# Optimization experiments

Measured on AMD Instinct MI355X. Metric: run time of the kernel, lower is better.

The kernel has to match this reference:

```python
import jax, jax.numpy as jnp
import numpy as np

HEADS = 8
DIM_HEAD = 128
EPS = 1e-5


def layer_norm(t, gamma):
    mu = jnp.mean(t, axis=-1, keepdims=True)
    var = jnp.var(t, axis=-1, keepdims=True)
    return (t - mu) / jnp.sqrt(var + EPS) * gamma


def setup_inputs() -> dict:
    key = jax.random.key(0)
    k1, k2, k3 = jax.random.split(key, 3)
    B, N, T, D = 16, 256, 4096, 1024
    img_queries = jax.random.normal(k1, (B, N, D), dtype=jnp.float32)
    x = jax.random.normal(k2, (B, T, D), dtype=jnp.float32)
    gamma_q = jnp.ones((D,), dtype=jnp.float32)
    gamma_x = jnp.ones((D,), dtype=jnp.float32)
    W_kv = jax.random.normal(k3, (D, 2 * DIM_HEAD), dtype=jnp.float32) * 0.02
    return {"img_queries": img_queries, "x": x, "gamma_q": gamma_q,
            "gamma_x": gamma_x, "W_kv": W_kv}


def reference(img_queries, x, gamma_q, gamma_x, W_kv):
    B, N, D = img_queries.shape
    scale = DIM_HEAD ** -0.5
    q_n = layer_norm(img_queries, gamma_q)            # [B,N,D]
    x_n = layer_norm(x, gamma_x)                      # [B,T,D]
    # b n (h d) -> b h n d
    q = q_n.reshape(B, N, HEADS, DIM_HEAD).transpose(0, 2, 1, 3)
    kv = x_n @ W_kv                                   # [B,T,2*dim_head]
    k = kv[..., :DIM_HEAD]                            # shared single K head; v chunk unused
    sim = jnp.einsum('bhid,bjd->bhij', q * scale, k)  # [B,H,N,T]
    sim = sim - jnp.max(sim, axis=-1, keepdims=True)
    attn = jax.nn.softmax(sim, axis=-1)
    out = jnp.einsum('bhij,bjf->bhif', attn, x_n)     # V = raw normed x, [B,H,N,D]
    # b h n f -> b (n h f)
    out = out.transpose(0, 2, 1, 3).reshape(B, N * HEADS * D)
    return out, attn
```

## Files before the change

### kernel.cpp

```cpp
#include <hip/hip_runtime.h>

typedef unsigned short u16;
typedef unsigned int u32;
typedef __attribute__((ext_vector_type(8))) short short8;
typedef __attribute__((ext_vector_type(4))) float f32x4;
typedef __attribute__((ext_vector_type(4))) unsigned int u32x4;

#define SCALE 0.08838834764831845f
#define OUT_ELEMS 33554432ull

__device__ __forceinline__ u16 f2b(float f) {
  u32 u = __float_as_uint(f);
  u32 r = u + 0x7fffu + ((u >> 16) & 1u);
  return (u16)(r >> 16);
}

__device__ __forceinline__ u32 cvtpk(float lo, float hi) {
  u32 r;
  asm("v_cvt_pk_bf16_f32 %0, %1, %2" : "=v"(r) : "v"(lo), "v"(hi));
  return r;
}

__device__ __forceinline__ void gload16(const void* g, void* l) {
  __builtin_amdgcn_global_load_lds((const __attribute__((address_space(1))) void*)g,
                                   (__attribute__((address_space(3))) void*)l, 16, 0, 0);
}

__device__ __forceinline__ uint2 shflx2(uint2 v, int m) {
  uint2 r;
  r.x = __shfl_xor(v.x, m, 64);
  r.y = __shfl_xor(v.y, m, 64);
  return r;
}

__global__ __launch_bounds__(256) void ln_rows(const float* __restrict__ in,
                                               const float* __restrict__ gamma,
                                               u16* __restrict__ out, float scale) {
  const int row = blockIdx.x;
  const int t = threadIdx.x;
  const float4 v = *(const float4*)(in + (size_t)row * 1024 + t * 4);
  float s = v.x + v.y + v.z + v.w;
  float q = v.x * v.x + v.y * v.y + v.z * v.z + v.w * v.w;
#pragma unroll
  for (int m = 32; m; m >>= 1) {
    s += __shfl_down(s, m);
    q += __shfl_down(q, m);
  }
  __shared__ float red[8];
  const int w = t >> 6;
  if ((t & 63) == 0) { red[w] = s; red[4 + w] = q; }
  __syncthreads();
  s = red[0] + red[1] + red[2] + red[3];
  q = red[4] + red[5] + red[6] + red[7];
  const float mu = s * (1.0f / 1024.0f);
  const float var = q * (1.0f / 1024.0f) - mu * mu;
  const float rs = rsqrtf(var + 1e-5f) * scale;
  const float4 g = *(const float4*)(gamma + t * 4);
  ushort4 o;
  o.x = f2b((v.x - mu) * rs * g.x);
  o.y = f2b((v.y - mu) * rs * g.y);
  o.z = f2b((v.z - mu) * rs * g.z);
  o.w = f2b((v.w - mu) * rs * g.w);
  *(ushort4*)(out + (size_t)row * 1024 + t * 4) = o;
}

__global__ __launch_bounds__(256) void cvt_w(const float* __restrict__ w, u16* __restrict__ wt) {
  const int n = blockIdx.x;
  const int t = threadIdx.x;
  const int d = t * 4;
  ushort4 o;
  o.x = f2b(w[(size_t)(d + 0) * 256 + n]);
  o.y = f2b(w[(size_t)(d + 1) * 256 + n]);
  o.z = f2b(w[(size_t)(d + 2) * 256 + n]);
  o.w = f2b(w[(size_t)(d + 3) * 256 + n]);
  *(ushort4*)(wt + (size_t)n * 1024 + d) = o;
}

__global__ __launch_bounds__(256) void transpose_xn(const u16* __restrict__ xn,
                                                    u16* __restrict__ xnt) {
  const int jt = blockIdx.x, dt = blockIdx.y, b = blockIdx.z;
  __shared__ u16 tile[64][72];
  const int t = threadIdx.x;
  const size_t src = ((size_t)b * 4096 + jt * 64) * 1024 + dt * 64;
#pragma unroll
  for (int p = 0; p < 2; ++p) {
    const int idx = t + 256 * p;
    const int j = idx >> 3, c = idx & 7;
    *(short8*)(&tile[j][c * 8]) = *(const short8*)(xn + src + (size_t)j * 1024 + c * 8);
  }
  __syncthreads();
  const size_t dst = ((size_t)b * 1024 + dt * 64) * 4096 + jt * 64;
#pragma unroll
  for (int p = 0; p < 2; ++p) {
    const int idx = t + 256 * p;
    const int d = idx >> 3, jj = idx & 7;
    short8 o;
#pragma unroll
    for (int e = 0; e < 8; ++e) o[e] = (short)tile[jj * 8 + e][d];
    *(short8*)(xnt + dst + (size_t)d * 4096 + jj * 8) = o;
  }
}

__global__ __launch_bounds__(256) void kgemm(const u16* __restrict__ xn,
                                             const u16* __restrict__ wt,
                                             u16* __restrict__ ks) {
  __shared__ u16 As[128 * 32];
  __shared__ u16 Bs[128 * 32];
  const int t = threadIdx.x;
  const int lane = t & 63, w = t >> 6;
  const int wm = w >> 1, wn = w & 1;
  const int j0 = blockIdx.x * 128;
  const int g = lane >> 4, r16 = lane & 15;
  f32x4 acc[4][4] = {};
  for (int k0 = 0; k0 < 1024; k0 += 32) {
    __syncthreads();
#pragma unroll
    for (int i = 0; i < 2; ++i) {
      const int seg = i * 4 + w;
      const int off = seg * 1024 + lane * 16;
      const int row = off >> 6;
      const int c = (off >> 4) & 3;
      const int sw = c ^ ((row >> 1) & 3);
      gload16(xn + ((size_t)(j0 + row)) * 1024 + k0 + sw * 8, (char*)As + seg * 1024);
      gload16(wt + ((size_t)row) * 1024 + k0 + sw * 8, (char*)Bs + seg * 1024);
    }
    __syncthreads();
    short8 a[4], bq[4];
#pragma unroll
    for (int mt = 0; mt < 4; ++mt) {
      const int row = wm * 64 + mt * 16 + r16;
      const int sw = g ^ ((row >> 1) & 3);
      a[mt] = *(const short8*)(As + row * 32 + sw * 8);
    }
#pragma unroll
    for (int nt = 0; nt < 4; ++nt) {
      const int row = wn * 64 + nt * 16 + r16;
      const int sw = g ^ ((row >> 1) & 3);
      bq[nt] = *(const short8*)(Bs + row * 32 + sw * 8);
    }
#pragma unroll
    for (int mt = 0; mt < 4; ++mt)
#pragma unroll
      for (int nt = 0; nt < 4; ++nt)
        acc[mt][nt] = __builtin_amdgcn_mfma_f32_16x16x32_bf16(a[mt], bq[nt], acc[mt][nt], 0, 0, 0);
  }
#pragma unroll
  for (int mt = 0; mt < 4; ++mt)
#pragma unroll
    for (int nt = 0; nt < 4; ++nt)
#pragma unroll
      for (int r = 0; r < 4; ++r) {
        const int j = j0 + wm * 64 + mt * 16 + g * 4 + r;
        const int n = wn * 64 + nt * 16 + r16;
        ks[(size_t)j * 128 + n] = f2b(acc[mt][nt][r]);
      }
}

__global__ __launch_bounds__(1024) void attn_kernel(const u16* __restrict__ qs,
                                                    const u16* __restrict__ ks,
                                                    float* __restrict__ attn,
                                                    u16* __restrict__ attnb) {
  const int blk = blockIdx.x;
  const int it = blk & 15, h = (blk >> 4) & 7, b = blk >> 7;
  const int i0 = it * 16;
  const int t = threadIdx.x;
  const int lane = t & 63, w = t >> 6;
  const int g = lane >> 4, r16 = lane & 15;
  __shared__ u16 Q[16 * 128];
  __shared__ float redm[256];
  __shared__ float reds[256];
  if (t < 256) {
    const int row = t >> 4, c = t & 15;
    const int sw = c ^ (row & 7);
    *(short8*)(Q + row * 128 + sw * 8) =
        *(const short8*)(qs + ((size_t)(b * 256 + i0 + row)) * 1024 + h * 128 + c * 8);
  }
  __syncthreads();
  short8 a[4];
#pragma unroll
  for (int kp = 0; kp < 4; ++kp) {
    const int c = kp * 4 + g;
    const int sw = c ^ (r16 & 7);
    a[kp] = *(const short8*)(Q + r16 * 128 + sw * 8);
  }
  const u16* kb = ks + (size_t)b * 4096 * 128;
  const int j0 = w * 256;
  f32x4 acc[16] = {};
#pragma unroll
  for (int kp = 0; kp < 4; ++kp) {
#pragma unroll
    for (int nt = 0; nt < 16; ++nt) {
      const short8 bv = *(const short8*)(kb + (size_t)(j0 + nt * 16 + r16) * 128 + kp * 32 + g * 8);
      acc[nt] = __builtin_amdgcn_mfma_f32_16x16x32_bf16(bv, a[kp], acc[nt], 0, 0, 0);
    }
  }
  float mx = acc[0][0];
#pragma unroll
  for (int nt = 0; nt < 16; ++nt)
#pragma unroll
    for (int r = 0; r < 4; ++r) mx = fmaxf(mx, acc[nt][r]);
  mx = fmaxf(mx, __shfl_xor(mx, 16));
  mx = fmaxf(mx, __shfl_xor(mx, 32));
  if (lane < 16) redm[w * 16 + lane] = mx;
  __syncthreads();
  float m = redm[r16];
#pragma unroll
  for (int w2 = 1; w2 < 16; ++w2) m = fmaxf(m, redm[w2 * 16 + r16]);
  float sm = 0.f;
#pragma unroll
  for (int nt = 0; nt < 16; ++nt)
#pragma unroll
    for (int r = 0; r < 4; ++r) {
      const float p = __expf(acc[nt][r] - m);
      acc[nt][r] = p;
      sm += p;
    }
  sm += __shfl_xor(sm, 16);
  sm += __shfl_xor(sm, 32);
  if (lane < 16) reds[w * 16 + lane] = sm;
  __syncthreads();
  float s = reds[r16];
#pragma unroll
  for (int w2 = 1; w2 < 16; ++w2) s += reds[w2 * 16 + r16];
  const float inv = 1.0f / s;
#pragma unroll
  for (int nt = 0; nt < 16; ++nt) acc[nt] *= inv;

  float* arow = attn + ((size_t)((b * 8 + h) * 256 + i0 + r16)) * 4096 + j0;
#pragma unroll
  for (int nt = 0; nt < 16; ++nt)
    *(f32x4*)(arow + nt * 16 + g * 4) = acc[nt];

  u16* brow = attnb + ((size_t)((b * 8 + h) * 256 + i0 + r16)) * 4096 + j0;
  const bool gb0 = (g & 1), gb1 = (g & 2);
#pragma unroll
  for (int q4 = 0; q4 < 4; ++q4) {
    uint2 X[4];
#pragma unroll
    for (int i = 0; i < 4; ++i) {
      const f32x4 v = acc[q4 * 4 + i];
      X[i] = make_uint2(cvtpk(v[0], v[1]), cvtpk(v[2], v[3]));
    }
#pragma unroll
    for (int k = 0; k < 2; ++k) {
      const uint2 aa = X[2 * k], bb = X[2 * k + 1];
      const uint2 sent = gb0 ? aa : bb;
      const uint2 recv = shflx2(sent, 16);
      X[2 * k] = gb0 ? recv : aa;
      X[2 * k + 1] = gb0 ? bb : recv;
    }
#pragma unroll
    for (int k = 0; k < 2; ++k) {
      const uint2 aa = X[k], bb = X[k + 2];
      const uint2 sent = gb1 ? aa : bb;
      const uint2 recv = shflx2(sent, 32);
      X[k] = gb1 ? recv : aa;
      X[k + 2] = gb1 ? bb : recv;
    }
    u16* bp = brow + q4 * 64 + g * 16;
    u32x4 o0 = {X[0].x, X[0].y, X[1].x, X[1].y};
    u32x4 o1 = {X[2].x, X[2].y, X[3].x, X[3].y};
    __builtin_nontemporal_store(o0, (u32x4*)bp);
    __builtin_nontemporal_store(o1, (u32x4*)(bp + 8));
  }
}

__global__ __launch_bounds__(512, 2) void ogemm256(const u16* __restrict__ attnb,
                                                   const u16* __restrict__ xnt,
                                                   float* __restrict__ out) {
  extern __shared__ u16 S[];
  const int orig = blockIdx.x;
  const int wid = (orig & 7) * 64 + (orig >> 3);
  const int b = wid >> 5, ft = (wid >> 3) & 3, h = wid & 7;
  const int t = threadIdx.x;
  const int lane = t & 63, w = t >> 6;
  const int wm = w >> 2, wn = w & 3;
  const int g = lane >> 4, r16 = lane & 15;
  const u16* Ab = attnb + ((size_t)(b * 8 + h) * 256) * 4096;
  const u16* Bb = xnt + ((size_t)b * 1024 + ft * 256) * 4096;

  int srow[4], scol[4];
#pragma unroll
  for (int seg = 0; seg < 4; ++seg) {
    const int gi = seg * 512 + t;
    srow[seg] = gi >> 3;
    scol[seg] = (((gi & 7) ^ ((gi >> 3) & 7)) * 8);
  }
  const int wuni = w * 1024;

#define OSTAGE(buf, k0)                                                         \
  do {                                                                          \
    _Pragma("unroll") for (int seg = 0; seg < 4; ++seg)                         \
        gload16(Ab + (size_t)srow[seg] * 4096 + (k0) + scol[seg],               \
                (char*)S + (buf)*32768 + seg * 8192 + wuni);                    \
    _Pragma("unroll") for (int seg = 0; seg < 4; ++seg)                         \
        gload16(Bb + (size_t)srow[seg] * 4096 + (k0) + scol[seg],               \
                (char*)S + 65536 + (buf)*32768 + seg * 8192 + wuni);            \
  } while (0)

  f32x4 acc[8][4] = {};
  OSTAGE(0, 0);
  OSTAGE(1, 64);
  asm volatile("s_waitcnt vmcnt(8)" ::: "memory");
  __builtin_amdgcn_s_barrier();

  for (int t64 = 0; t64 < 64; ++t64) {
    const int buf = t64 & 1;
    const char* A0 = (const char*)S + buf * 32768;
    const char* B0 = (const char*)S + 65536 + buf * 32768;
    short8 af[8], bf[4];
#pragma unroll
    for (int mt = 0; mt < 8; ++mt) {
      const int row = wm * 128 + mt * 16 + r16;
      af[mt] = *(const short8*)(A0 + row * 128 + ((g ^ (row & 7)) * 16));
    }
#pragma unroll
    for (int nt = 0; nt < 4; ++nt) {
      const int row = wn * 64 + nt * 16 + r16;
      bf[nt] = *(const short8*)(B0 + row * 128 + ((g ^ (row & 7)) * 16));
    }
    asm volatile("s_waitcnt lgkmcnt(0)" ::: "memory");
    __builtin_amdgcn_sched_barrier(0);
    __builtin_amdgcn_s_setprio(1);
#pragma unroll
    for (int mt = 0; mt < 8; ++mt)
#pragma unroll
      for (int nt = 0; nt < 4; ++nt)
        acc[mt][nt] = __builtin_amdgcn_mfma_f32_16x16x32_bf16(af[mt], bf[nt], acc[mt][nt], 0, 0, 0);
    __builtin_amdgcn_s_setprio(0);
#pragma unroll
    for (int mt = 0; mt < 8; ++mt) {
      const int row = wm * 128 + mt * 16 + r16;
      af[mt] = *(const short8*)(A0 + row * 128 + (((4 + g) ^ (row & 7)) * 16));
    }
#pragma unroll
    for (int nt = 0; nt < 4; ++nt) {
      const int row = wn * 64 + nt * 16 + r16;
      bf[nt] = *(const short8*)(B0 + row * 128 + (((4 + g) ^ (row & 7)) * 16));
    }
    asm volatile("s_waitcnt lgkmcnt(0)" ::: "memory");
    __builtin_amdgcn_sched_barrier(0);
    __builtin_amdgcn_s_barrier();
    if (t64 + 2 < 64) OSTAGE(buf, (t64 + 2) * 64);
    __builtin_amdgcn_s_setprio(1);
#pragma unroll
    for (int mt = 0; mt < 8; ++mt)
#pragma unroll
      for (int nt = 0; nt < 4; ++nt)
        acc[mt][nt] = __builtin_amdgcn_mfma_f32_16x16x32_bf16(af[mt], bf[nt], acc[mt][nt], 0, 0, 0);
    __builtin_amdgcn_s_setprio(0);
    if (t64 + 2 < 64)
      asm volatile("s_waitcnt vmcnt(8)" ::: "memory");
    else if (t64 == 62)
      asm volatile("s_waitcnt vmcnt(0)" ::: "memory");
    __builtin_amdgcn_s_barrier();
  }
#undef OSTAGE

  float* ob = out + (size_t)b * 2097152 + (size_t)h * 1024;
#pragma unroll
  for (int mt = 0; mt < 8; ++mt)
#pragma unroll
    for (int nt = 0; nt < 4; ++nt)
#pragma unroll
      for (int r = 0; r < 4; ++r) {
        const int i = wm * 128 + mt * 16 + g * 4 + r;
        const int f = ft * 256 + wn * 64 + nt * 16 + r16;
        ob[(size_t)i * 8192 + f] = acc[mt][nt][r];
      }
}

extern "C" void kernel_launch(void* const* d_in, const int* in_sizes, int n_in,
                              void* d_out, int out_size, void* d_ws, size_t ws_size,
                              hipStream_t stream) {
  const float* img_q = (const float*)d_in[0];
  const float* x = (const float*)d_in[1];
  const float* gamma_q = (const float*)d_in[2];
  const float* gamma_x = (const float*)d_in[3];
  const float* wkv = (const float*)d_in[4];

  float* out_f = (float*)d_out;
  float* attn_f = out_f + OUT_ELEMS;

  u16* xn = (u16*)attn_f;
  u16* qsb = (u16*)out_f;
  u16* wtb = qsb + 4194304;
  u16* ksb = wtb + 131072;
  u16* xnt = (u16*)d_ws;
  u16* attnb = xnt + 67108864;

  if (ws_size < (size_t)402653184) return;

  (void)hipFuncSetAttribute((const void*)ogemm256,
                            hipFuncAttributeMaxDynamicSharedMemorySize, 131072);

  ln_rows<<<65536, 256, 0, stream>>>(x, gamma_x, xn, 1.0f);
  ln_rows<<<4096, 256, 0, stream>>>(img_q, gamma_q, qsb, SCALE);
  cvt_w<<<128, 256, 0, stream>>>(wkv, wtb);
  transpose_xn<<<dim3(64, 16, 16), 256, 0, stream>>>(xn, xnt);
  kgemm<<<512, 256, 0, stream>>>(xn, wtb, ksb);
  attn_kernel<<<2048, 1024, 0, stream>>>(qsb, ksb, attn_f, attnb);
  ogemm256<<<512, 512, 131072, stream>>>(attnb, xnt, out_f);
}
```

Baseline: 886.4 us.

## Write fp32 attn output from bf16 LDS tiles inside output GEMM

The softmax kernel no longer stores the fp32 attention matrix. It now writes only the bf16 copy. The output GEMM blocks with ft==0 read the bf16 attention tile already staged in LDS, widen it to fp32 and store it with nontemporal writes, overlapping that traffic with the MFMA loop. The attn kernel also gets a block-index swizzle, and the ogemm occupancy hint is dropped. The returned attn values are now bf16-rounded, which loses precision, and the extra stores fall on a quarter of the GEMM blocks, which may unbalance them.

```diff
diff --git a/kernel.cpp b/kernel.cpp
--- a/kernel.cpp
+++ b/kernel.cpp
@@ -158,9 +158,9 @@
 
 __global__ __launch_bounds__(1024) void attn_kernel(const u16* __restrict__ qs,
                                                     const u16* __restrict__ ks,
-                                                    float* __restrict__ attn,
                                                     u16* __restrict__ attnb) {
-  const int blk = blockIdx.x;
+  const int orig = blockIdx.x;
+  const int blk = (orig & 7) * 256 + (orig >> 3);
   const int it = blk & 15, h = (blk >> 4) & 7, b = blk >> 7;
   const int i0 = it * 16;
   const int t = threadIdx.x;
@@ -226,11 +226,6 @@
 #pragma unroll
   for (int nt = 0; nt < 16; ++nt) acc[nt] *= inv;
 
-  float* arow = attn + ((size_t)((b * 8 + h) * 256 + i0 + r16)) * 4096 + j0;
-#pragma unroll
-  for (int nt = 0; nt < 16; ++nt)
-    *(f32x4*)(arow + nt * 16 + g * 4) = acc[nt];
-
   u16* brow = attnb + ((size_t)((b * 8 + h) * 256 + i0 + r16)) * 4096 + j0;
   const bool gb0 = (g & 1), gb1 = (g & 2);
 #pragma unroll
@@ -265,9 +260,10 @@
   }
 }
 
-__global__ __launch_bounds__(512, 2) void ogemm256(const u16* __restrict__ attnb,
-                                                   const u16* __restrict__ xnt,
-                                                   float* __restrict__ out) {
+__global__ __launch_bounds__(512) void ogemm256(const u16* __restrict__ attnb,
+                                                const u16* __restrict__ xnt,
+                                                float* __restrict__ out,
+                                                float* __restrict__ attn) {
   extern __shared__ u16 S[];
   const int orig = blockIdx.x;
   const int wid = (orig & 7) * 64 + (orig >> 3);
@@ -278,6 +274,9 @@
   const int g = lane >> 4, r16 = lane & 15;
   const u16* Ab = attnb + ((size_t)(b * 8 + h) * 256) * 4096;
   const u16* Bb = xnt + ((size_t)b * 1024 + ft * 256) * 4096;
+  const bool wrA = (ft == 0);
+  float* attn_out = attn + ((size_t)(b * 8 + h) * 256) * 4096;
+  const int awr = t >> 1, awh = t & 1;
 
   int srow[4], scol[4];
 #pragma unroll
@@ -338,8 +337,28 @@
       const int row = wn * 64 + nt * 16 + r16;
       bf[nt] = *(const short8*)(B0 + row * 128 + (((4 + g) ^ (row & 7)) * 16));
     }
+    short8 wv[4];
+    if (wrA) {
+#pragma unroll
+      for (int c2 = 0; c2 < 4; ++c2)
+        wv[c2] = *(const short8*)(A0 + awr * 128 + (((awh * 4 + c2) ^ (awr & 7)) * 16));
+    }
     asm volatile("s_waitcnt lgkmcnt(0)" ::: "memory");
     __builtin_amdgcn_sched_barrier(0);
+    if (wrA) {
+      float* dst = attn_out + (size_t)awr * 4096 + t64 * 64 + awh * 32;
+#pragma unroll
+      for (int c2 = 0; c2 < 4; ++c2) {
+        f32x4 lo, hi;
+#pragma unroll
+        for (int e = 0; e < 4; ++e) {
+          lo[e] = __uint_as_float(((u32)(u16)wv[c2][e]) << 16);
+          hi[e] = __uint_as_float(((u32)(u16)wv[c2][4 + e]) << 16);
+        }
+        __builtin_nontemporal_store(lo, (f32x4*)(dst + c2 * 8));
+        __builtin_nontemporal_store(hi, (f32x4*)(dst + c2 * 8 + 4));
+      }
+    }
     __builtin_amdgcn_s_barrier();
     if (t64 + 2 < 64) OSTAGE(buf, (t64 + 2) * 64);
     __builtin_amdgcn_s_setprio(1);
@@ -399,6 +418,6 @@
   cvt_w<<<128, 256, 0, stream>>>(wkv, wtb);
   transpose_xn<<<dim3(64, 16, 16), 256, 0, stream>>>(xn, xnt);
   kgemm<<<512, 256, 0, stream>>>(xn, wtb, ksb);
-  attn_kernel<<<2048, 1024, 0, stream>>>(qsb, ksb, attn_f, attnb);
-  ogemm256<<<512, 512, 131072, stream>>>(attnb, xnt, out_f);
-}
+  attn_kernel<<<2048, 1024, 0, stream>>>(qsb, ksb, attnb);
+  ogemm256<<<512, 512, 131072, stream>>>(attnb, xnt, out_f, attn_f);
+}
```

After: 1.954 ms. 120% more time.
